# Kernel optimization log

Hardware: AMD Instinct MI355X
Metric: run time of the kernel (lower is better)

The kernel has to match this reference:

```python
import jax, jax.numpy as jnp
import numpy as np

N = 16384          # num nodes (128 graphs x 128 turbines)
E = 262144         # edges before self loops
TURBINE_NUM = 128
D_IN = 512         # input_dim (= 2*hidden_dim1)
H1 = 256           # hidden_dim1
H2 = 256           # hidden_dim2
NEG_SLOPE = 0.2    # PyG GATConv default leaky relu slope


def _glorot(key, shape, fan_in):
    return jax.random.normal(key, shape, dtype=jnp.float32) / np.sqrt(fan_in)


def setup_inputs() -> dict:
    key = jax.random.key(0)
    ks = jax.random.split(key, 12)
    x = jax.random.normal(ks[0], (N, H2), dtype=jnp.float32)
    adj = jax.random.randint(ks[1], (2, E), 0, N, dtype=jnp.int64)
    # fc: Linear(hidden_dim2 -> hidden_dim1); stored as [in, out]
    W_fc = _glorot(ks[2], (H2, H1), H2)
    b_fc = jnp.zeros((H1,), dtype=jnp.float32)
    # gat1: GATConv(H1 -> H1, heads=2, concat)
    W1 = _glorot(ks[3], (H1, 2 * H1), H1)
    a1_src = _glorot(ks[4], (2, H1), H1)
    a1_dst = _glorot(ks[5], (2, H1), H1)
    b1 = jnp.zeros((2 * H1,), dtype=jnp.float32)
    # gat2: GATConv(D_IN -> D_IN, heads=1, concat)
    W2 = _glorot(ks[6], (D_IN, D_IN), D_IN)
    a2_src = _glorot(ks[7], (1, D_IN), D_IN)
    a2_dst = _glorot(ks[8], (1, D_IN), D_IN)
    b2 = jnp.zeros((D_IN,), dtype=jnp.float32)
    return dict(x=x, adj=adj, W_fc=W_fc, b_fc=b_fc, W1=W1, a1_src=a1_src,
                a1_dst=a1_dst, b1=b1, W2=W2, a2_src=a2_src, a2_dst=a2_dst, b2=b2)


def gat_conv(x, src, dst, W, a_src, a_dst, bias, heads, out_ch):
    """PyG GATConv (eval mode, self loops already in src/dst)."""
    n = x.shape[0]
    h = (x @ W).reshape(n, heads, out_ch)                 # [N,H,C]
    al_s = jnp.einsum('nhc,hc->nh', h, a_src)             # [N,H]
    al_d = jnp.einsum('nhc,hc->nh', h, a_dst)
    e = jax.nn.leaky_relu(al_s[src] + al_d[dst], NEG_SLOPE)  # [E,H]
    # segment softmax over incoming edges per destination node
    e_max = jax.ops.segment_max(e, dst, num_segments=n)
    e_exp = jnp.exp(e - e_max[dst])
    denom = jax.ops.segment_sum(e_exp, dst, num_segments=n)
    alpha = e_exp / (denom[dst] + 1e-16)                  # [E,H]
    msg = h[src] * alpha[:, :, None]                      # [E,H,C]
    out = jax.ops.segment_sum(msg, dst, num_segments=n)   # [N,H,C]
    return out.reshape(n, heads * out_ch) + bias


def reference(x, adj, W_fc, b_fc, W1, a1_src, a1_dst, b1, W2, a2_src, a2_dst, b2):
    # add self loops (PyG GATConv default)
    loops = jnp.arange(N, dtype=adj.dtype)
    src = jnp.concatenate([adj[0], loops])
    dst = jnp.concatenate([adj[1], loops])
    h = jax.nn.relu(x @ W_fc + b_fc)                      # fc + ReLU
    h = gat_conv(h, src, dst, W1, a1_src, a1_dst, b1, heads=2, out_ch=H1)
    h = jax.nn.relu(h)
    h = gat_conv(h, src, dst, W2, a2_src, a2_dst, b2, heads=1, out_ch=D_IN)
    y = jax.nn.relu(h)
    return y.reshape(-1, TURBINE_NUM, y.shape[1])         # [128,128,512]
```

## Files before the change

kernel.cpp:

```cpp
#include <hip/hip_runtime.h>

#define N_NODES 16384
#define N_EDGES 262144
#define E_TOT   (N_EDGES + N_NODES)
#define NEG_SLOPE 0.2f

typedef __attribute__((ext_vector_type(8))) short short8;
typedef __attribute__((ext_vector_type(4))) float floatx4;
typedef __attribute__((ext_vector_type(4))) int intx4;

__device__ __forceinline__ float bf2f(ushort u) {
    return __uint_as_float(((unsigned)u) << 16);
}
__device__ __forceinline__ ushort f2bf(float f) {
    unsigned u = __float_as_uint(f);
    u += 0x7fffu + ((u >> 16) & 1u);
    return (ushort)(u >> 16);
}
__device__ __forceinline__ float leaky(float x) {
    return x > 0.f ? x : NEG_SLOPE * x;
}

__device__ __forceinline__ void load_lds16(const void* g, void* l) {
    __builtin_amdgcn_global_load_lds(
        (const __attribute__((address_space(1))) unsigned int*)g,
        (__attribute__((address_space(3))) unsigned int*)l, 16, 0, 0);
}

#define PREP_CAST   524288
#define PREP_T0     (PREP_CAST)
#define PREP_T1     (PREP_T0 + 65536)
#define PREP_T2     (PREP_T1 + 131072)
#define PREP_Z      (PREP_T2 + 262144)
#define PREP_TOT    (PREP_Z + 4096)

__global__ __launch_bounds__(256) void k_prep(const float* __restrict__ x,
                                              ushort* __restrict__ xb,
                                              const float* __restrict__ Wfc,
                                              ushort* __restrict__ WfcT,
                                              const float* __restrict__ W1,
                                              ushort* __restrict__ W1T,
                                              const float* __restrict__ W2,
                                              ushort* __restrict__ W2T,
                                              int* __restrict__ counts) {
    int idx = blockIdx.x * 256 + threadIdx.x;
    if (idx < PREP_CAST) {
        floatx4 v0 = *(const floatx4*)(x + (size_t)idx * 8);
        floatx4 v1 = *(const floatx4*)(x + (size_t)idx * 8 + 4);
        short8 r;
        r[0] = (short)f2bf(v0[0]); r[1] = (short)f2bf(v0[1]);
        r[2] = (short)f2bf(v0[2]); r[3] = (short)f2bf(v0[3]);
        r[4] = (short)f2bf(v1[0]); r[5] = (short)f2bf(v1[1]);
        r[6] = (short)f2bf(v1[2]); r[7] = (short)f2bf(v1[3]);
        *(short8*)(xb + (size_t)idx * 8) = r;
    } else if (idx < PREP_T1) {
        int t = idx - PREP_T0;
        int k = t >> 8, n = t & 255;
        WfcT[n * 256 + k] = f2bf(Wfc[t]);
    } else if (idx < PREP_T2) {
        int t = idx - PREP_T1;
        int k = t >> 9, n = t & 511;
        W1T[n * 256 + k] = f2bf(W1[t]);
    } else if (idx < PREP_Z) {
        int t = idx - PREP_T2;
        int k = t >> 9, n = t & 511;
        W2T[n * 512 + k] = f2bf(W2[t]);
    } else if (idx < PREP_TOT) {
        int t = idx - PREP_Z;
        *(intx4*)(counts + t * 4) = (intx4){0, 0, 0, 0};
    }
}

__global__ __launch_bounds__(256) void k_hist(const int* __restrict__ adj,
                                              int* __restrict__ counts) {
    int e = blockIdx.x * 256 + threadIdx.x;
    if (e < E_TOT) {
        int d = (e < N_EDGES) ? adj[N_EDGES + e] : (e - N_EDGES);
        atomicAdd(&counts[d], 1);
    }
}

__global__ __launch_bounds__(1024) void k_scan(const int* __restrict__ counts,
                                               int* __restrict__ offs,
                                               int* __restrict__ cursor) {
    __shared__ int wsum[16];
    int t = threadIdx.x, lane = t & 63, w = t >> 6;
    int local[16];
    int tot = 0;
#pragma unroll
    for (int i = 0; i < 16; i++) {
        local[i] = tot;
        tot += counts[t * 16 + i];
    }
    int incl = tot;
#pragma unroll
    for (int d = 1; d < 64; d <<= 1) {
        int v = __shfl_up(incl, d, 64);
        if (lane >= d) incl += v;
    }
    if (lane == 63) wsum[w] = incl;
    __syncthreads();
    if (w == 0) {
        int v = (lane < 16) ? wsum[lane] : 0;
#pragma unroll
        for (int d = 1; d < 16; d <<= 1) {
            int u = __shfl_up(v, d, 64);
            if (lane >= d) v += u;
        }
        if (lane < 16) wsum[lane] = v;
    }
    __syncthreads();
    int base = ((w == 0) ? 0 : wsum[w - 1]) + incl - tot;
#pragma unroll
    for (int i = 0; i < 16; i++) {
        int o = base + local[i];
        offs[t * 16 + i] = o;
        cursor[t * 16 + i] = o;
    }
    if (t == 1023) offs[N_NODES] = wsum[15];
}

__global__ __launch_bounds__(256) void k_scatter(const int* __restrict__ adj,
                                                 int* __restrict__ cursor,
                                                 int* __restrict__ esrc) {
    int e = blockIdx.x * 256 + threadIdx.x;
    if (e < E_TOT) {
        int s, d;
        if (e < N_EDGES) { s = adj[e]; d = adj[N_EDGES + e]; }
        else             { s = e - N_EDGES; d = s; }
        int pos = atomicAdd(&cursor[d], 1);
        esrc[pos] = s;
    }
}

#define GM 128
#define GN 128
#define GK 64

__global__ __launch_bounds__(256) void gemm128(const ushort* __restrict__ A,
                                               const ushort* __restrict__ BT,
                                               const float* __restrict__ bias,
                                               ushort* __restrict__ C,
                                               int M, int Nc, int K, int relu) {
    __shared__ ushort As[GM * GK];
    __shared__ ushort Bs[GN * GK];
    int tid = threadIdx.x, wave = tid >> 6, lane = tid & 63;
    int quad = lane >> 4, l16 = lane & 15;
    int bm = blockIdx.x * GM, bn = blockIdx.y * GN;
    int wm = (wave & 1) * 64, wn = (wave >> 1) * 64;

    floatx4 acc[4][4];
#pragma unroll
    for (int mi = 0; mi < 4; mi++)
#pragma unroll
        for (int ni = 0; ni < 4; ni++)
            acc[mi][ni] = (floatx4){0.f, 0.f, 0.f, 0.f};

    int lrow = lane >> 3;
    int lcol = (lane & 7) * 8;
    const ushort* pA = A + (size_t)(bm + wave * 32 + lrow) * K + lcol;
    const ushort* pB = BT + (size_t)(bn + wave * 32 + lrow) * K + lcol;
    ushort* lA = &As[(wave * 32) * GK];
    ushort* lB = &Bs[(wave * 32) * GK];

    for (int kb = 0; kb < K; kb += GK) {
#pragma unroll
        for (int t = 0; t < 4; t++) {
            load_lds16(pA + (size_t)(t * 8) * K + kb, lA + t * 8 * GK);
            load_lds16(pB + (size_t)(t * 8) * K + kb, lB + t * 8 * GK);
        }
        __syncthreads();

#pragma unroll
        for (int kk = 0; kk < GK; kk += 32) {
            short8 af[4], bf[4];
#pragma unroll
            for (int mi = 0; mi < 4; mi++)
                af[mi] = *(const short8*)&As[(wm + mi * 16 + l16) * GK + kk + quad * 8];
#pragma unroll
            for (int ni = 0; ni < 4; ni++)
                bf[ni] = *(const short8*)&Bs[(wn + ni * 16 + l16) * GK + kk + quad * 8];
#pragma unroll
            for (int mi = 0; mi < 4; mi++)
#pragma unroll
                for (int ni = 0; ni < 4; ni++)
                    acc[mi][ni] = __builtin_amdgcn_mfma_f32_16x16x32_bf16(
                        af[mi], bf[ni], acc[mi][ni], 0, 0, 0);
        }
        __syncthreads();
    }

#pragma unroll
    for (int mi = 0; mi < 4; mi++) {
        int row = bm + wm + mi * 16 + quad * 4;
#pragma unroll
        for (int ni = 0; ni < 4; ni++) {
            int col = bn + wn + ni * 16 + l16;
            float bv = bias ? bias[col] : 0.f;
#pragma unroll
            for (int i = 0; i < 4; i++) {
                float v = acc[mi][ni][i] + bv;
                if (relu) v = fmaxf(v, 0.f);
                C[(size_t)(row + i) * Nc + col] = f2bf(v);
            }
        }
    }
}

__global__ __launch_bounds__(256) void k_dots(const ushort* __restrict__ h,
                                              const float* __restrict__ asrc,
                                              const float* __restrict__ adst,
                                              float* __restrict__ als,
                                              float* __restrict__ ald,
                                              int heads) {
    int wave = threadIdx.x >> 6, lane = threadIdx.x & 63;
    int n = blockIdx.x * 4 + wave;
    const ushort* hr = h + (size_t)n * 512;
    int c = lane * 8;
    short8 hv = *(const short8*)(hr + c);
    floatx4 s0 = *(const floatx4*)(asrc + c);
    floatx4 s1 = *(const floatx4*)(asrc + c + 4);
    floatx4 d0 = *(const floatx4*)(adst + c);
    floatx4 d1 = *(const floatx4*)(adst + c + 4);
    float ps = 0.f, pd = 0.f;
#pragma unroll
    for (int j = 0; j < 4; j++) {
        float hf0 = bf2f((ushort)hv[j]);
        float hf1 = bf2f((ushort)hv[j + 4]);
        ps += hf0 * s0[j] + hf1 * s1[j];
        pd += hf0 * d0[j] + hf1 * d1[j];
    }
    int w = (heads == 2) ? 32 : 64;
    for (int m = 1; m < w; m <<= 1) {
        ps += __shfl_xor(ps, m, 64);
        pd += __shfl_xor(pd, m, 64);
    }
    if (heads == 2) {
        if (lane == 0)  { als[n * 2]     = ps; ald[n * 2]     = pd; }
        if (lane == 32) { als[n * 2 + 1] = ps; ald[n * 2 + 1] = pd; }
    } else {
        if (lane == 0)  { als[n] = ps; ald[n] = pd; }
    }
}

__global__ __launch_bounds__(256) void k_agg(const ushort* __restrict__ h,
                                             const float* __restrict__ als,
                                             const float* __restrict__ ald,
                                             const int* __restrict__ offs,
                                             const int* __restrict__ esrc,
                                             const float* __restrict__ bias,
                                             ushort* __restrict__ outb,
                                             float* __restrict__ outf,
                                             int heads) {
    __shared__ float sPart[2][512];
    int wave = threadIdx.x >> 6, lane = threadIdx.x & 63;
    int nib = wave >> 1;
    int sub = wave & 1;
    int n = blockIdx.x * 2 + nib;
    int base = offs[n];
    int deg  = offs[n + 1] - base;

    int myhead = (heads == 2) ? (lane >> 5) : 0;
    int c = (heads == 2) ? (myhead * 256 + (lane & 31) * 8) : lane * 8;

    float aldh0 = ald[n * heads];
    float aldh1 = (heads == 2) ? ald[n * heads + 1] : 0.f;

    float m0 = -1e30f, m1 = -1e30f;
    for (int cb = 0; cb < deg; cb += 64) {
        int i = cb + lane;
        if (i < deg) {
            int s = esrc[base + i];
            m0 = fmaxf(m0, leaky(als[s * heads] + aldh0));
            if (heads == 2) m1 = fmaxf(m1, leaky(als[s * 2 + 1] + aldh1));
        }
    }
#pragma unroll
    for (int msk = 1; msk < 64; msk <<= 1) {
        m0 = fmaxf(m0, __shfl_xor(m0, msk, 64));
        m1 = fmaxf(m1, __shfl_xor(m1, msk, 64));
    }

    float s0 = 0.f, s1 = 0.f;
    for (int cb = 0; cb < deg; cb += 64) {
        int i = cb + lane;
        if (i < deg) {
            int s = esrc[base + i];
            s0 += __expf(leaky(als[s * heads] + aldh0) - m0);
            if (heads == 2) s1 += __expf(leaky(als[s * 2 + 1] + aldh1) - m1);
        }
    }
#pragma unroll
    for (int msk = 1; msk < 64; msk <<= 1) {
        s0 += __shfl_xor(s0, msk, 64);
        s1 += __shfl_xor(s1, msk, 64);
    }
    float inv0 = 1.f / (s0 + 1e-16f);
    float inv1 = 1.f / (s1 + 1e-16f);

    float acc[8];
#pragma unroll
    for (int q = 0; q < 8; q++) acc[q] = 0.f;
    const ushort* hc = h + c;

    for (int cb = 0; cb < deg; cb += 128) {
        int ei = cb + lane * 2 + sub;
        int sv = 0;
        float p0 = 0.f, p1 = 0.f;
        if (ei < deg) {
            sv = esrc[base + ei];
            p0 = __expf(leaky(als[sv * heads] + aldh0) - m0) * inv0;
            if (heads == 2) p1 = __expf(leaky(als[sv * 2 + 1] + aldh1) - m1) * inv1;
        }
        int cnt = min(128, deg - cb);
        int nw = (cnt > sub) ? ((cnt - sub + 1) >> 1) : 0;
        int j = 0;
        for (; j + 4 <= nw; j += 4) {
            int sj0 = __shfl(sv, j, 64);
            int sj1 = __shfl(sv, j + 1, 64);
            int sj2 = __shfl(sv, j + 2, 64);
            int sj3 = __shfl(sv, j + 3, 64);
            float a00 = __shfl(p0, j, 64),     a01 = __shfl(p1, j, 64);
            float a10 = __shfl(p0, j + 1, 64), a11 = __shfl(p1, j + 1, 64);
            float a20 = __shfl(p0, j + 2, 64), a21 = __shfl(p1, j + 2, 64);
            float a30 = __shfl(p0, j + 3, 64), a31 = __shfl(p1, j + 3, 64);
            float al0 = myhead ? a01 : a00;
            float al1 = myhead ? a11 : a10;
            float al2 = myhead ? a21 : a20;
            float al3 = myhead ? a31 : a30;
            short8 h0v = *(const short8*)(hc + (size_t)sj0 * 512);
            short8 h1v = *(const short8*)(hc + (size_t)sj1 * 512);
            short8 h2v = *(const short8*)(hc + (size_t)sj2 * 512);
            short8 h3v = *(const short8*)(hc + (size_t)sj3 * 512);
#pragma unroll
            for (int q = 0; q < 8; q++) {
                acc[q] += al0 * bf2f((ushort)h0v[q]);
                acc[q] += al1 * bf2f((ushort)h1v[q]);
                acc[q] += al2 * bf2f((ushort)h2v[q]);
                acc[q] += al3 * bf2f((ushort)h3v[q]);
            }
        }
        for (; j < nw; j++) {
            int s = __shfl(sv, j, 64);
            float a0 = __shfl(p0, j, 64), a1 = __shfl(p1, j, 64);
            float al = myhead ? a1 : a0;
            short8 hv = *(const short8*)(hc + (size_t)s * 512);
#pragma unroll
            for (int q = 0; q < 8; q++) acc[q] += al * bf2f((ushort)hv[q]);
        }
    }

    if (sub == 1) {
#pragma unroll
        for (int q = 0; q < 8; q++) sPart[nib][c + q] = acc[q];
    }
    __syncthreads();
    if (sub == 0) {
        float v[8];
#pragma unroll
        for (int q = 0; q < 8; q++)
            v[q] = fmaxf(acc[q] + sPart[nib][c + q] + bias[c + q], 0.f);
        if (outf) {
            float* op = outf + (size_t)n * 512 + c;
            *(floatx4*)op       = (floatx4){v[0], v[1], v[2], v[3]};
            *(floatx4*)(op + 4) = (floatx4){v[4], v[5], v[6], v[7]};
        } else {
            short8 r;
#pragma unroll
            for (int q = 0; q < 8; q++) r[q] = (short)f2bf(v[q]);
            *(short8*)(outb + (size_t)n * 512 + c) = r;
        }
    }
}

extern "C" void kernel_launch(void* const* d_in, const int* in_sizes, int n_in,
                              void* d_out, int out_size, void* d_ws, size_t ws_size,
                              hipStream_t stream) {
    const float* x   = (const float*)d_in[0];
    const int*   adj = (const int*)d_in[1];
    const float* Wfc = (const float*)d_in[2];
    const float* bfc = (const float*)d_in[3];
    const float* W1  = (const float*)d_in[4];
    const float* a1s = (const float*)d_in[5];
    const float* a1d = (const float*)d_in[6];
    const float* b1  = (const float*)d_in[7];
    const float* W2  = (const float*)d_in[8];
    const float* a2s = (const float*)d_in[9];
    const float* a2d = (const float*)d_in[10];
    const float* b2  = (const float*)d_in[11];
    float* out = (float*)d_out;

    char* ws = (char*)d_ws;
    size_t off = 0;
    auto alloc = [&](size_t bytes) -> void* {
        void* p = ws + off;
        off += (bytes + 255) & ~(size_t)255;
        return p;
    };
    ushort* xb   = (ushort*)alloc((size_t)N_NODES * 256 * 2);
    ushort* h0b  = (ushort*)alloc((size_t)N_NODES * 256 * 2);
    ushort* h1b  = (ushort*)alloc((size_t)N_NODES * 512 * 2);
    ushort* g1b  = (ushort*)alloc((size_t)N_NODES * 512 * 2);
    int* counts  = (int*)alloc(N_NODES * 4);
    int* offs    = (int*)alloc((N_NODES + 1) * 4);
    int* cursor  = (int*)alloc(N_NODES * 4);
    int* esrc    = (int*)alloc(E_TOT * 4);
    ushort* WfcT = (ushort*)alloc(256 * 256 * 2);
    ushort* W1T  = (ushort*)alloc(512 * 256 * 2);
    ushort* W2T  = (ushort*)alloc(512 * 512 * 2);
    float* als1  = (float*)alloc(N_NODES * 2 * 4);
    float* ald1  = (float*)alloc(N_NODES * 2 * 4);
    float* als2  = (float*)alloc(N_NODES * 4);
    float* ald2  = (float*)alloc(N_NODES * 4);

    k_prep<<<PREP_TOT / 256, 256, 0, stream>>>(x, xb, Wfc, WfcT, W1, W1T, W2, W2T,
                                               counts);

    k_hist<<<(E_TOT + 255) / 256, 256, 0, stream>>>(adj, counts);
    k_scan<<<1, 1024, 0, stream>>>(counts, offs, cursor);
    k_scatter<<<(E_TOT + 255) / 256, 256, 0, stream>>>(adj, cursor, esrc);

    gemm128<<<dim3(N_NODES / GM, 256 / GN), 256, 0, stream>>>(xb, WfcT, bfc, h0b,
                                                              N_NODES, 256, 256, 1);
    gemm128<<<dim3(N_NODES / GM, 512 / GN), 256, 0, stream>>>(h0b, W1T, nullptr, h1b,
                                                              N_NODES, 512, 256, 0);
    k_dots<<<N_NODES / 4, 256, 0, stream>>>(h1b, a1s, a1d, als1, ald1, 2);
    k_agg<<<N_NODES / 2, 256, 0, stream>>>(h1b, als1, ald1, offs, esrc, b1,
                                           g1b, nullptr, 2);

    gemm128<<<dim3(N_NODES / GM, 512 / GN), 256, 0, stream>>>(g1b, W2T, nullptr, h1b,
                                                              N_NODES, 512, 512, 0);
    k_dots<<<N_NODES / 4, 256, 0, stream>>>(h1b, a2s, a2d, als2, ald2, 1);
    k_agg<<<N_NODES / 2, 256, 0, stream>>>(h1b, als2, ald2, offs, esrc, b2,
                                           nullptr, out, 1);
}
```

Measured before the change: 271.3 us.

## Aggregate one node per wave with 8-way gather unroll and packed FMA

The aggregation kernel now assigns one destination node per wave, four per block, instead of splitting each node's edges across two waves and combining them through shared memory and a block barrier. The inner gather loop is unrolled to eight independent row loads, to keep more memory requests in flight, and accumulates into float2 vectors so the compiler can use packed FMA. This removes the LDS reduction and __syncthreads, at the cost of less parallelism per node for high-degree nodes and higher register pressure.

```diff
diff --git a/kernel.cpp b/kernel.cpp
--- a/kernel.cpp
+++ b/kernel.cpp
@@ -7,6 +7,7 @@
 
 typedef __attribute__((ext_vector_type(8))) short short8;
 typedef __attribute__((ext_vector_type(4))) float floatx4;
+typedef __attribute__((ext_vector_type(2))) float floatx2;
 typedef __attribute__((ext_vector_type(4))) int intx4;
 
 __device__ __forceinline__ float bf2f(ushort u) {
@@ -252,11 +253,8 @@
                                              ushort* __restrict__ outb,
                                              float* __restrict__ outf,
                                              int heads) {
-    __shared__ float sPart[2][512];
     int wave = threadIdx.x >> 6, lane = threadIdx.x & 63;
-    int nib = wave >> 1;
-    int sub = wave & 1;
-    int n = blockIdx.x * 2 + nib;
+    int n = blockIdx.x * 4 + wave;
     int base = offs[n];
     int deg  = offs[n + 1] - base;
 
@@ -298,78 +296,83 @@
     float inv0 = 1.f / (s0 + 1e-16f);
     float inv1 = 1.f / (s1 + 1e-16f);
 
-    float acc[8];
-#pragma unroll
-    for (int q = 0; q < 8; q++) acc[q] = 0.f;
+    floatx2 acc2[4];
+#pragma unroll
+    for (int q = 0; q < 4; q++) acc2[q] = (floatx2){0.f, 0.f};
     const ushort* hc = h + c;
 
-    for (int cb = 0; cb < deg; cb += 128) {
-        int ei = cb + lane * 2 + sub;
+    for (int cb = 0; cb < deg; cb += 64) {
+        int i = cb + lane;
         int sv = 0;
         float p0 = 0.f, p1 = 0.f;
-        if (ei < deg) {
-            sv = esrc[base + ei];
+        if (i < deg) {
+            sv = esrc[base + i];
             p0 = __expf(leaky(als[sv * heads] + aldh0) - m0) * inv0;
             if (heads == 2) p1 = __expf(leaky(als[sv * 2 + 1] + aldh1) - m1) * inv1;
         }
-        int cnt = min(128, deg - cb);
-        int nw = (cnt > sub) ? ((cnt - sub + 1) >> 1) : 0;
+        int cnt = min(64, deg - cb);
         int j = 0;
-        for (; j + 4 <= nw; j += 4) {
-            int sj0 = __shfl(sv, j, 64);
-            int sj1 = __shfl(sv, j + 1, 64);
-            int sj2 = __shfl(sv, j + 2, 64);
-            int sj3 = __shfl(sv, j + 3, 64);
-            float a00 = __shfl(p0, j, 64),     a01 = __shfl(p1, j, 64);
-            float a10 = __shfl(p0, j + 1, 64), a11 = __shfl(p1, j + 1, 64);
-            float a20 = __shfl(p0, j + 2, 64), a21 = __shfl(p1, j + 2, 64);
-            float a30 = __shfl(p0, j + 3, 64), a31 = __shfl(p1, j + 3, 64);
-            float al0 = myhead ? a01 : a00;
-            float al1 = myhead ? a11 : a10;
-            float al2 = myhead ? a21 : a20;
-            float al3 = myhead ? a31 : a30;
-            short8 h0v = *(const short8*)(hc + (size_t)sj0 * 512);
-            short8 h1v = *(const short8*)(hc + (size_t)sj1 * 512);
-            short8 h2v = *(const short8*)(hc + (size_t)sj2 * 512);
-            short8 h3v = *(const short8*)(hc + (size_t)sj3 * 512);
-#pragma unroll
-            for (int q = 0; q < 8; q++) {
-                acc[q] += al0 * bf2f((ushort)h0v[q]);
-                acc[q] += al1 * bf2f((ushort)h1v[q]);
-                acc[q] += al2 * bf2f((ushort)h2v[q]);
-                acc[q] += al3 * bf2f((ushort)h3v[q]);
+        for (; j + 8 <= cnt; j += 8) {
+            int sj[8];
+            float alv[8];
+            const uint* rp[8];
+#pragma unroll
+            for (int u = 0; u < 8; u++) {
+                sj[u] = __shfl(sv, j + u, 64);
+                float a0 = __shfl(p0, j + u, 64);
+                float a1 = __shfl(p1, j + u, 64);
+                alv[u] = myhead ? a1 : a0;
+                rp[u] = (const uint*)(hc + (size_t)sj[u] * 512);
             }
-        }
-        for (; j < nw; j++) {
+            uint4 rv[8];
+#pragma unroll
+            for (int u = 0; u < 8; u++) rv[u] = *(const uint4*)rp[u];
+#pragma unroll
+            for (int u = 0; u < 8; u++) {
+                floatx2 al2 = (floatx2){alv[u], alv[u]};
+                uint w0 = rv[u].x, w1 = rv[u].y, w2 = rv[u].z, w3 = rv[u].w;
+                floatx2 f0 = (floatx2){bf2f((ushort)(w0 & 0xffffu)), bf2f((ushort)(w0 >> 16))};
+                floatx2 f1 = (floatx2){bf2f((ushort)(w1 & 0xffffu)), bf2f((ushort)(w1 >> 16))};
+                floatx2 f2 = (floatx2){bf2f((ushort)(w2 & 0xffffu)), bf2f((ushort)(w2 >> 16))};
+                floatx2 f3 = (floatx2){bf2f((ushort)(w3 & 0xffffu)), bf2f((ushort)(w3 >> 16))};
+                acc2[0] += al2 * f0;
+                acc2[1] += al2 * f1;
+                acc2[2] += al2 * f2;
+                acc2[3] += al2 * f3;
+            }
+        }
+        for (; j < cnt; j++) {
             int s = __shfl(sv, j, 64);
             float a0 = __shfl(p0, j, 64), a1 = __shfl(p1, j, 64);
             float al = myhead ? a1 : a0;
-            short8 hv = *(const short8*)(hc + (size_t)s * 512);
-#pragma unroll
-            for (int q = 0; q < 8; q++) acc[q] += al * bf2f((ushort)hv[q]);
-        }
-    }
-
-    if (sub == 1) {
-#pragma unroll
-        for (int q = 0; q < 8; q++) sPart[nib][c + q] = acc[q];
-    }
-    __syncthreads();
-    if (sub == 0) {
-        float v[8];
-#pragma unroll
-        for (int q = 0; q < 8; q++)
-            v[q] = fmaxf(acc[q] + sPart[nib][c + q] + bias[c + q], 0.f);
-        if (outf) {
-            float* op = outf + (size_t)n * 512 + c;
-            *(floatx4*)op       = (floatx4){v[0], v[1], v[2], v[3]};
-            *(floatx4*)(op + 4) = (floatx4){v[4], v[5], v[6], v[7]};
-        } else {
-            short8 r;
-#pragma unroll
-            for (int q = 0; q < 8; q++) r[q] = (short)f2bf(v[q]);
-            *(short8*)(outb + (size_t)n * 512 + c) = r;
-        }
+            floatx2 al2 = (floatx2){al, al};
+            uint4 rv = *(const uint4*)(hc + (size_t)s * 512);
+            floatx2 f0 = (floatx2){bf2f((ushort)(rv.x & 0xffffu)), bf2f((ushort)(rv.x >> 16))};
+            floatx2 f1 = (floatx2){bf2f((ushort)(rv.y & 0xffffu)), bf2f((ushort)(rv.y >> 16))};
+            floatx2 f2 = (floatx2){bf2f((ushort)(rv.z & 0xffffu)), bf2f((ushort)(rv.z >> 16))};
+            floatx2 f3 = (floatx2){bf2f((ushort)(rv.w & 0xffffu)), bf2f((ushort)(rv.w >> 16))};
+            acc2[0] += al2 * f0;
+            acc2[1] += al2 * f1;
+            acc2[2] += al2 * f2;
+            acc2[3] += al2 * f3;
+        }
+    }
+
+    float v[8];
+#pragma unroll
+    for (int q = 0; q < 4; q++) {
+        v[2 * q]     = fmaxf(acc2[q][0] + bias[c + 2 * q], 0.f);
+        v[2 * q + 1] = fmaxf(acc2[q][1] + bias[c + 2 * q + 1], 0.f);
+    }
+    if (outf) {
+        float* op = outf + (size_t)n * 512 + c;
+        *(floatx4*)op       = (floatx4){v[0], v[1], v[2], v[3]};
+        *(floatx4*)(op + 4) = (floatx4){v[4], v[5], v[6], v[7]};
+    } else {
+        short8 r;
+#pragma unroll
+        for (int q = 0; q < 8; q++) r[q] = (short)f2bf(v[q]);
+        *(short8*)(outb + (size_t)n * 512 + c) = r;
     }
 }
 
@@ -425,12 +428,12 @@
     gemm128<<<dim3(N_NODES / GM, 512 / GN), 256, 0, stream>>>(h0b, W1T, nullptr, h1b,
                                                               N_NODES, 512, 256, 0);
     k_dots<<<N_NODES / 4, 256, 0, stream>>>(h1b, a1s, a1d, als1, ald1, 2);
-    k_agg<<<N_NODES / 2, 256, 0, stream>>>(h1b, als1, ald1, offs, esrc, b1,
+    k_agg<<<N_NODES / 4, 256, 0, stream>>>(h1b, als1, ald1, offs, esrc, b1,
                                            g1b, nullptr, 2);
 
     gemm128<<<dim3(N_NODES / GM, 512 / GN), 256, 0, stream>>>(g1b, W2T, nullptr, h1b,
                                                               N_NODES, 512, 512, 0);
     k_dots<<<N_NODES / 4, 256, 0, stream>>>(h1b, a2s, a2d, als2, ald2, 1);
-    k_agg<<<N_NODES / 2, 256, 0, stream>>>(h1b, als2, ald2, offs, esrc, b2,
+    k_agg<<<N_NODES / 4, 256, 0, stream>>>(h1b, als2, ald2, offs, esrc, b2,
                                            nullptr, out, 1);
 }
```

Result: no change. 274.4 us (+1.2%).
